# Kernel optimization log

Hardware: AMD Instinct MI355X
Metric: run time of the kernel (lower is better)

The kernel has to match this reference:

```python
import jax, jax.numpy as jnp
import numpy as np

N_NODES = 50000


def setup_inputs() -> dict:
    key = jax.random.key(0)
    k1, k2, k3, k4, k5, k6 = jax.random.split(key, 6)
    feature = jax.random.normal(k1, (N_NODES, 128), dtype=jnp.float32)
    norm = jax.random.uniform(k2, (N_NODES, 1), dtype=jnp.float32)
    W = jax.random.normal(k3, (128, 128), dtype=jnp.float32) * 0.05
    b = jax.random.normal(k4, (128,), dtype=jnp.float32) * 0.05
    src = jax.random.randint(k5, (600000,), 0, N_NODES, dtype=jnp.int32)
    dst = jax.random.randint(k6, (600000,), 0, N_NODES, dtype=jnp.int32)
    return {"feature": feature, "norm": norm, "W": W, "b": b, "src": src, "dst": dst}


def reference(feature, norm, W, b, src, dst):
    n = feature.shape[0]
    # message: h_src * norm_src, gathered per edge  [E, d]
    msg = feature[src] * norm[src]
    # scatter-sum into destination nodes, then scale by norm_dst
    accum = jax.ops.segment_sum(msg, dst, num_segments=n) * norm
    # DGL semantics: nodes with zero in-degree keep their original feature
    in_deg = jax.ops.segment_sum(jnp.ones((dst.shape[0],), dtype=jnp.float32), dst, num_segments=n)
    h = jnp.where(in_deg[:, None] > 0, accum, feature)
    # node apply: linear + relu
    return jax.nn.relu(h @ W.T + b)
```

## Files before the change

kernel.cpp:

```cpp
#include <hip/hip_runtime.h>

#define N_NODES 50000
#define N_EDGES 600000
#define D 128
#define CAP 64

typedef __attribute__((ext_vector_type(8))) short bf16x8;
typedef __attribute__((ext_vector_type(4))) float f32x4;
typedef __attribute__((ext_vector_type(4))) unsigned short ushort4v;

__device__ inline unsigned int f2bf_u(float f) {
    unsigned int u = __builtin_bit_cast(unsigned int, f);
    return (u + 0x7FFFu + ((u >> 16) & 1u)) >> 16;
}
__device__ inline unsigned int pack2(float lo, float hi) {
    return f2bf_u(lo) | (f2bf_u(hi) << 16);
}
__device__ inline float bf_lo(unsigned int u) {
    return __builtin_bit_cast(float, u << 16);
}
__device__ inline float bf_hi(unsigned int u) {
    return __builtin_bit_cast(float, u & 0xFFFF0000u);
}

__global__ __launch_bounds__(256) void init_kernel(
    const float* __restrict__ feat, const float* __restrict__ norm,
    const float* __restrict__ W,
    unsigned short* __restrict__ g, unsigned short* __restrict__ Wb,
    int* __restrict__ cursor)
{
    const int b = blockIdx.x, t = threadIdx.x;
    if (b < 3125) {
        int gid = b * 256 + t;
        int row = gid >> 4;
        int c8  = (gid & 15) * 8;
        float nr = norm[row];
        float4 f0 = *reinterpret_cast<const float4*>(feat + (size_t)row * D + c8);
        float4 f1 = *reinterpret_cast<const float4*>(feat + (size_t)row * D + c8 + 4);
        uint4 o;
        o.x = pack2(f0.x * nr, f0.y * nr);
        o.y = pack2(f0.z * nr, f0.w * nr);
        o.z = pack2(f1.x * nr, f1.y * nr);
        o.w = pack2(f1.z * nr, f1.w * nr);
        *reinterpret_cast<uint4*>(g + (size_t)row * D + c8) = o;
    } else if (b < 3141) {
        int j = (b - 3125) * 256 + t;
        float4 w = *reinterpret_cast<const float4*>(W + (size_t)j * 4);
        ushort4 o;
        o.x = (unsigned short)f2bf_u(w.x);
        o.y = (unsigned short)f2bf_u(w.y);
        o.z = (unsigned short)f2bf_u(w.z);
        o.w = (unsigned short)f2bf_u(w.w);
        *reinterpret_cast<ushort4*>(Wb + (size_t)j * 4) = o;
    } else {
        int idx = (b - 3141) * 256 + t;
        if (idx < 12500) *reinterpret_cast<int4*>(cursor + idx * 4) = make_int4(0, 0, 0, 0);
    }
}

__global__ __launch_bounds__(256) void fill_kernel(
    const int* __restrict__ src, const int* __restrict__ dst,
    int* __restrict__ cursor, unsigned short* __restrict__ csr16, int E)
{
    int e = blockIdx.x * blockDim.x + threadIdx.x;
    if (e < E) {
        int d = dst[e];
        int slot = atomicAdd(&cursor[d], 1);
        if (slot < CAP) csr16[((size_t)d << 6) + slot] = (unsigned short)src[e];
    }
}

__global__ __launch_bounds__(256) void gather_mfma(
    const unsigned short* __restrict__ g,
    const float* __restrict__ feat, const float* __restrict__ norm,
    const int* __restrict__ cursor,
    const unsigned short* __restrict__ csr16,
    const unsigned short* __restrict__ Wb,
    const float* __restrict__ bias,
    float* __restrict__ out)
{
    __shared__ __align__(16) unsigned short hsh[16 * 136];
    const int t    = threadIdx.x;
    const int w    = t >> 6;
    const int lane = t & 63;
    const int kg   = lane >> 4;
    const int mr   = lane & 15;
    const int nbase = blockIdx.x * 16;

    const int ln   = w * 4 + kg;
    const int node = nbase + ln;
    const int deg  = min(cursor[node], CAP);
    const int base = node << 6;

    float a0 = 0.f, a1 = 0.f, a2 = 0.f, a3 = 0.f;
    float a4 = 0.f, a5 = 0.f, a6 = 0.f, a7 = 0.f;
    const unsigned short* gcol = g + mr * 8;

    int i = 0;
    for (; i + 4 <= deg; i += 4) {
        ushort4v ix = *reinterpret_cast<const ushort4v*>(csr16 + base + i);
        uint4 v0 = *reinterpret_cast<const uint4*>(gcol + (size_t)ix[0] * D);
        uint4 v1 = *reinterpret_cast<const uint4*>(gcol + (size_t)ix[1] * D);
        uint4 v2 = *reinterpret_cast<const uint4*>(gcol + (size_t)ix[2] * D);
        uint4 v3 = *reinterpret_cast<const uint4*>(gcol + (size_t)ix[3] * D);
        a0 += bf_lo(v0.x) + bf_lo(v1.x) + bf_lo(v2.x) + bf_lo(v3.x);
        a1 += bf_hi(v0.x) + bf_hi(v1.x) + bf_hi(v2.x) + bf_hi(v3.x);
        a2 += bf_lo(v0.y) + bf_lo(v1.y) + bf_lo(v2.y) + bf_lo(v3.y);
        a3 += bf_hi(v0.y) + bf_hi(v1.y) + bf_hi(v2.y) + bf_hi(v3.y);
        a4 += bf_lo(v0.z) + bf_lo(v1.z) + bf_lo(v2.z) + bf_lo(v3.z);
        a5 += bf_hi(v0.z) + bf_hi(v1.z) + bf_hi(v2.z) + bf_hi(v3.z);
        a6 += bf_lo(v0.w) + bf_lo(v1.w) + bf_lo(v2.w) + bf_lo(v3.w);
        a7 += bf_hi(v0.w) + bf_hi(v1.w) + bf_hi(v2.w) + bf_hi(v3.w);
    }
    for (; i < deg; ++i) {
        unsigned short s0 = csr16[base + i];
        uint4 v0 = *reinterpret_cast<const uint4*>(gcol + (size_t)s0 * D);
        a0 += bf_lo(v0.x); a1 += bf_hi(v0.x);
        a2 += bf_lo(v0.y); a3 += bf_hi(v0.y);
        a4 += bf_lo(v0.z); a5 += bf_hi(v0.z);
        a6 += bf_lo(v0.w); a7 += bf_hi(v0.w);
    }

    if (deg == 0) {
        float4 f0 = *reinterpret_cast<const float4*>(feat + (size_t)node * D + mr * 8);
        float4 f1 = *reinterpret_cast<const float4*>(feat + (size_t)node * D + mr * 8 + 4);
        a0 = f0.x; a1 = f0.y; a2 = f0.z; a3 = f0.w;
        a4 = f1.x; a5 = f1.y; a6 = f1.z; a7 = f1.w;
    } else {
        float nd = norm[node];
        a0 *= nd; a1 *= nd; a2 *= nd; a3 *= nd;
        a4 *= nd; a5 *= nd; a6 *= nd; a7 *= nd;
    }
    uint4 o;
    o.x = pack2(a0, a1);
    o.y = pack2(a2, a3);
    o.z = pack2(a4, a5);
    o.w = pack2(a6, a7);
    *reinterpret_cast<uint4*>(&hsh[ln * 136 + mr * 8]) = o;
    __syncthreads();

    bf16x8 fa0 = *reinterpret_cast<const bf16x8*>(&hsh[mr * 136 + kg * 8]);
    bf16x8 fa1 = *reinterpret_cast<const bf16x8*>(&hsh[mr * 136 + kg * 8 + 32]);
    bf16x8 fa2 = *reinterpret_cast<const bf16x8*>(&hsh[mr * 136 + kg * 8 + 64]);
    bf16x8 fa3 = *reinterpret_cast<const bf16x8*>(&hsh[mr * 136 + kg * 8 + 96]);

    const int orow0 = nbase + kg * 4;
    #pragma unroll
    for (int nn = 0; nn < 2; ++nn) {
        const int n0 = w * 2 + nn;
        const size_t bbase = (size_t)(n0 * 16 + mr) * D + kg * 8;
        bf16x8 b0 = *reinterpret_cast<const bf16x8*>(Wb + bbase);
        bf16x8 b1 = *reinterpret_cast<const bf16x8*>(Wb + bbase + 32);
        bf16x8 b2 = *reinterpret_cast<const bf16x8*>(Wb + bbase + 64);
        bf16x8 b3 = *reinterpret_cast<const bf16x8*>(Wb + bbase + 96);
        f32x4 acc = {0.f, 0.f, 0.f, 0.f};
        acc = __builtin_amdgcn_mfma_f32_16x16x32_bf16(fa0, b0, acc, 0, 0, 0);
        acc = __builtin_amdgcn_mfma_f32_16x16x32_bf16(fa1, b1, acc, 0, 0, 0);
        acc = __builtin_amdgcn_mfma_f32_16x16x32_bf16(fa2, b2, acc, 0, 0, 0);
        acc = __builtin_amdgcn_mfma_f32_16x16x32_bf16(fa3, b3, acc, 0, 0, 0);

        const int c = n0 * 16 + mr;
        const float bv = bias[c];
        #pragma unroll
        for (int j = 0; j < 4; ++j) {
            float r = acc[j] + bv;
            out[(size_t)(orow0 + j) * D + c] = r > 0.f ? r : 0.f;
        }
    }
}

extern "C" void kernel_launch(void* const* d_in, const int* in_sizes, int n_in,
                              void* d_out, int out_size, void* d_ws, size_t ws_size,
                              hipStream_t stream) {
    const float* feat = (const float*)d_in[0];
    const float* norm = (const float*)d_in[1];
    const float* W    = (const float*)d_in[2];
    const float* bias = (const float*)d_in[3];
    const int*   src  = (const int*)d_in[4];
    const int*   dst  = (const int*)d_in[5];
    float* out = (float*)d_out;

    char* ws = (char*)d_ws;
    unsigned short* g      = (unsigned short*)ws;
    int*            cursor = (int*)(ws + (size_t)N_NODES * D * sizeof(unsigned short));
    unsigned short* csr16  = (unsigned short*)(cursor + N_NODES);
    unsigned short* Wb     = csr16 + (size_t)N_NODES * CAP;

    const int egrid = (N_EDGES + 255) / 256;
    init_kernel<<<3190, 256, 0, stream>>>(feat, norm, W, g, Wb, cursor);
    fill_kernel<<<egrid, 256, 0, stream>>>(src, dst, cursor, csr16, N_EDGES);
    gather_mfma<<<N_NODES / 16, 256, 0, stream>>>(g, feat, norm, cursor, csr16, Wb, bias, out);
}
```

Measured before the change: 79.65 us.

## Overlap edge scatter with feature conversion and double-buffer gather loads

Splits setup so the small W conversion and cursor zeroing run first, then merges the edge atomic fill and the feature-to-bf16 conversion into one launch so the two independent workloads run concurrently. The gather loop is software-pipelined with two register buffers, so the next four neighbour rows load while the current four accumulate. An occupancy hint of 8 blocks per CU is added to launch_bounds. The extra live registers may conflict with that occupancy target and cause spills.

```diff
diff --git a/kernel.cpp b/kernel.cpp
--- a/kernel.cpp
+++ b/kernel.cpp
@@ -23,15 +23,42 @@
     return __builtin_bit_cast(float, u & 0xFFFF0000u);
 }
 
-__global__ __launch_bounds__(256) void init_kernel(
-    const float* __restrict__ feat, const float* __restrict__ norm,
-    const float* __restrict__ W,
-    unsigned short* __restrict__ g, unsigned short* __restrict__ Wb,
+__global__ __launch_bounds__(256) void setup_kernel(
+    const float* __restrict__ W, unsigned short* __restrict__ Wb,
     int* __restrict__ cursor)
 {
     const int b = blockIdx.x, t = threadIdx.x;
-    if (b < 3125) {
-        int gid = b * 256 + t;
+    if (b < 16) {
+        int j = b * 256 + t;
+        float4 w = *reinterpret_cast<const float4*>(W + (size_t)j * 4);
+        ushort4 o;
+        o.x = (unsigned short)f2bf_u(w.x);
+        o.y = (unsigned short)f2bf_u(w.y);
+        o.z = (unsigned short)f2bf_u(w.z);
+        o.w = (unsigned short)f2bf_u(w.w);
+        *reinterpret_cast<ushort4*>(Wb + (size_t)j * 4) = o;
+    } else {
+        int idx = (b - 16) * 256 + t;
+        if (idx < 12500) *reinterpret_cast<int4*>(cursor + idx * 4) = make_int4(0, 0, 0, 0);
+    }
+}
+
+__global__ __launch_bounds__(256) void prefill_kernel(
+    const int* __restrict__ src, const int* __restrict__ dst,
+    const float* __restrict__ feat, const float* __restrict__ norm,
+    int* __restrict__ cursor, unsigned short* __restrict__ csr16,
+    unsigned short* __restrict__ g)
+{
+    const int b = blockIdx.x, t = threadIdx.x;
+    if (b < 2344) {
+        int e = b * 256 + t;
+        if (e < N_EDGES) {
+            int d = dst[e];
+            int slot = atomicAdd(&cursor[d], 1);
+            if (slot < CAP) csr16[((size_t)d << 6) + slot] = (unsigned short)src[e];
+        }
+    } else {
+        int gid = (b - 2344) * 256 + t;
         int row = gid >> 4;
         int c8  = (gid & 15) * 8;
         float nr = norm[row];
@@ -43,34 +70,28 @@
         o.z = pack2(f1.x * nr, f1.y * nr);
         o.w = pack2(f1.z * nr, f1.w * nr);
         *reinterpret_cast<uint4*>(g + (size_t)row * D + c8) = o;
-    } else if (b < 3141) {
-        int j = (b - 3125) * 256 + t;
-        float4 w = *reinterpret_cast<const float4*>(W + (size_t)j * 4);
-        ushort4 o;
-        o.x = (unsigned short)f2bf_u(w.x);
-        o.y = (unsigned short)f2bf_u(w.y);
-        o.z = (unsigned short)f2bf_u(w.z);
-        o.w = (unsigned short)f2bf_u(w.w);
-        *reinterpret_cast<ushort4*>(Wb + (size_t)j * 4) = o;
-    } else {
-        int idx = (b - 3141) * 256 + t;
-        if (idx < 12500) *reinterpret_cast<int4*>(cursor + idx * 4) = make_int4(0, 0, 0, 0);
-    }
-}
-
-__global__ __launch_bounds__(256) void fill_kernel(
-    const int* __restrict__ src, const int* __restrict__ dst,
-    int* __restrict__ cursor, unsigned short* __restrict__ csr16, int E)
-{
-    int e = blockIdx.x * blockDim.x + threadIdx.x;
-    if (e < E) {
-        int d = dst[e];
-        int slot = atomicAdd(&cursor[d], 1);
-        if (slot < CAP) csr16[((size_t)d << 6) + slot] = (unsigned short)src[e];
-    }
-}
-
-__global__ __launch_bounds__(256) void gather_mfma(
+    }
+}
+
+#define LOADB(bb, r0, r1, r2, r3) { \
+    ushort4v ix = *reinterpret_cast<const ushort4v*>(csr16 + base + (bb) * 4); \
+    r0 = *reinterpret_cast<const uint4*>(gcol + (size_t)ix[0] * D); \
+    r1 = *reinterpret_cast<const uint4*>(gcol + (size_t)ix[1] * D); \
+    r2 = *reinterpret_cast<const uint4*>(gcol + (size_t)ix[2] * D); \
+    r3 = *reinterpret_cast<const uint4*>(gcol + (size_t)ix[3] * D); \
+}
+#define ACCB(r0, r1, r2, r3) { \
+    a0 += bf_lo(r0.x) + bf_lo(r1.x) + bf_lo(r2.x) + bf_lo(r3.x); \
+    a1 += bf_hi(r0.x) + bf_hi(r1.x) + bf_hi(r2.x) + bf_hi(r3.x); \
+    a2 += bf_lo(r0.y) + bf_lo(r1.y) + bf_lo(r2.y) + bf_lo(r3.y); \
+    a3 += bf_hi(r0.y) + bf_hi(r1.y) + bf_hi(r2.y) + bf_hi(r3.y); \
+    a4 += bf_lo(r0.z) + bf_lo(r1.z) + bf_lo(r2.z) + bf_lo(r3.z); \
+    a5 += bf_hi(r0.z) + bf_hi(r1.z) + bf_hi(r2.z) + bf_hi(r3.z); \
+    a6 += bf_lo(r0.w) + bf_lo(r1.w) + bf_lo(r2.w) + bf_lo(r3.w); \
+    a7 += bf_hi(r0.w) + bf_hi(r1.w) + bf_hi(r2.w) + bf_hi(r3.w); \
+}
+
+__global__ __launch_bounds__(256, 8) void gather_mfma(
     const unsigned short* __restrict__ g,
     const float* __restrict__ feat, const float* __restrict__ norm,
     const int* __restrict__ cursor,
@@ -96,23 +117,19 @@
     float a4 = 0.f, a5 = 0.f, a6 = 0.f, a7 = 0.f;
     const unsigned short* gcol = g + mr * 8;
 
-    int i = 0;
-    for (; i + 4 <= deg; i += 4) {
-        ushort4v ix = *reinterpret_cast<const ushort4v*>(csr16 + base + i);
-        uint4 v0 = *reinterpret_cast<const uint4*>(gcol + (size_t)ix[0] * D);
-        uint4 v1 = *reinterpret_cast<const uint4*>(gcol + (size_t)ix[1] * D);
-        uint4 v2 = *reinterpret_cast<const uint4*>(gcol + (size_t)ix[2] * D);
-        uint4 v3 = *reinterpret_cast<const uint4*>(gcol + (size_t)ix[3] * D);
-        a0 += bf_lo(v0.x) + bf_lo(v1.x) + bf_lo(v2.x) + bf_lo(v3.x);
-        a1 += bf_hi(v0.x) + bf_hi(v1.x) + bf_hi(v2.x) + bf_hi(v3.x);
-        a2 += bf_lo(v0.y) + bf_lo(v1.y) + bf_lo(v2.y) + bf_lo(v3.y);
-        a3 += bf_hi(v0.y) + bf_hi(v1.y) + bf_hi(v2.y) + bf_hi(v3.y);
-        a4 += bf_lo(v0.z) + bf_lo(v1.z) + bf_lo(v2.z) + bf_lo(v3.z);
-        a5 += bf_hi(v0.z) + bf_hi(v1.z) + bf_hi(v2.z) + bf_hi(v3.z);
-        a6 += bf_lo(v0.w) + bf_lo(v1.w) + bf_lo(v2.w) + bf_lo(v3.w);
-        a7 += bf_hi(v0.w) + bf_hi(v1.w) + bf_hi(v2.w) + bf_hi(v3.w);
-    }
-    for (; i < deg; ++i) {
+    const int nb = deg >> 2;
+    uint4 x0, x1, x2, x3, y0, y1, y2, y3;
+
+    if (nb > 0) LOADB(0, x0, x1, x2, x3);
+    for (int b = 0; b + 2 <= nb; b += 2) {
+        LOADB(b + 1, y0, y1, y2, y3);
+        ACCB(x0, x1, x2, x3);
+        if (b + 2 < nb) LOADB(b + 2, x0, x1, x2, x3);
+        ACCB(y0, y1, y2, y3);
+    }
+    if (nb & 1) ACCB(x0, x1, x2, x3);
+
+    for (int i = nb * 4; i < deg; ++i) {
         unsigned short s0 = csr16[base + i];
         uint4 v0 = *reinterpret_cast<const uint4*>(gcol + (size_t)s0 * D);
         a0 += bf_lo(v0.x); a1 += bf_hi(v0.x);
@@ -186,8 +203,7 @@
     unsigned short* csr16  = (unsigned short*)(cursor + N_NODES);
     unsigned short* Wb     = csr16 + (size_t)N_NODES * CAP;
 
-    const int egrid = (N_EDGES + 255) / 256;
-    init_kernel<<<3190, 256, 0, stream>>>(feat, norm, W, g, Wb, cursor);
-    fill_kernel<<<egrid, 256, 0, stream>>>(src, dst, cursor, csr16, N_EDGES);
+    setup_kernel<<<65, 256, 0, stream>>>(W, Wb, cursor);
+    prefill_kernel<<<2344 + 3125, 256, 0, stream>>>(src, dst, feat, norm, cursor, csr16, g);
     gather_mfma<<<N_NODES / 16, 256, 0, stream>>>(g, feat, norm, cursor, csr16, Wb, bias, out);
 }
```

Measured after the change: 111.4 us. +39.9%, slower.
